# Kernel tuning notes

Measured on AMD Instinct MI355X. Metric: run time of the kernel, lower is better.

The kernel has to match this reference:

```python
import jax, jax.numpy as jnp
import numpy as np

B, LP, LQ, H = 16, 1024, 1024, 1024


def setup_inputs() -> dict:
    key = jax.random.key(0)
    k1, k2, k3 = jax.random.split(key, 3)
    p = jax.random.normal(k1, (B, LP, H), dtype=jnp.float32)
    q = jax.random.normal(k2, (B, LQ, H), dtype=jnp.float32)
    # Dense(hidden_size) kernel + bias (glorot-ish scale)
    W_key = jax.random.normal(k3, (H, H), dtype=jnp.float32) / np.sqrt(H)
    b_key = jnp.zeros((H,), dtype=jnp.float32)
    return {"p": p, "q": q, "W_key": W_key, "b_key": b_key}


def reference(p, q, W_key, b_key):
    # keys = Dense(q): [B, LQ, H]
    keys = jnp.einsum("bqh,hk->bqk", q, W_key) + b_key
    # attention scores p @ keys^T (no scaling): [B, LP, LQ]
    scores = jnp.einsum("bph,bqh->bpq", p, keys)
    attn = jax.nn.softmax(scores, axis=-1)
    # q reused as values; relu on output: [B, LP, H]
    out = jax.nn.relu(jnp.einsum("bpq,bqh->bph", attn, q))
    return out
```

## Files before the change

kernel.cpp:

```cpp
#include <hip/hip_runtime.h>
#include <hip/hip_bf16.h>

#define B_N 16
#define LP_N 1024
#define LQ_N 1024
#define H_N 1024

typedef unsigned short u16;
typedef __attribute__((ext_vector_type(8))) _Float16 f16x8;
typedef __attribute__((ext_vector_type(4))) float f32x4;

__device__ __forceinline__ u16 f2h(float x) {
    _Float16 h = (_Float16)x;
    return *(u16*)&h;
}
__device__ __forceinline__ float h2f(u16 u) {
    _Float16 h;
    *(u16*)&h = u;
    return (float)h;
}

__device__ __forceinline__ void load_lds16(const u16* g, u16* l) {
    __builtin_amdgcn_global_load_lds(
        (const __attribute__((address_space(1))) void*)g,
        (__attribute__((address_space(3))) void*)l, 16, 0, 0);
}

#define MFMA_F16(a, b, c) __builtin_amdgcn_mfma_f32_16x16x32_f16(a, b, c, 0, 0, 0)
#define VMW0()  asm volatile("s_waitcnt vmcnt(0)" ::: "memory")
#define VMW4()  asm volatile("s_waitcnt vmcnt(4)" ::: "memory")
#define LGKM8() asm volatile("s_waitcnt lgkmcnt(8)" ::: "memory")
#define LGKM0() asm volatile("s_waitcnt lgkmcnt(0)" ::: "memory")
#define SCHB()  __builtin_amdgcn_sched_barrier(0)
#define SBAR()  __builtin_amdgcn_s_barrier()

template<bool SPLIT, int EPI>
__launch_bounds__(512, 2)
__global__ void gemm2t(const u16* __restrict__ Ahi, const u16* __restrict__ Alo,
                       const u16* __restrict__ Bm,
                       const float* __restrict__ bias,
                       float* __restrict__ Cf, u16* __restrict__ Ch,
                       int N, int gn, int gmn,
                       long long sA, long long sB, long long sC)
{
    constexpr int REG  = 8192;
    constexpr int O_AL = REG;
    constexpr int O_B  = SPLIT ? 2 * REG : REG;
    constexpr int BUF  = SPLIT ? 3 * REG : 2 * REG;
    __shared__ __align__(16) u16 lds[2 * BUF];

    const int tid  = threadIdx.x;
    const int lane = tid & 63;
    const int wv   = tid >> 6;
    const int wr   = wv >> 2, wc = wv & 3;

    const int d   = blockIdx.x;
    const int cpx = gridDim.x >> 3;
    const int swz = (d & 7) * cpx + (d >> 3);
    const long long z = swz / gmn;
    const int r_  = swz % gmn;
    const int bm  = (r_ / gn) * 256;
    const int bn  = (r_ % gn) * 256;

    const char* pAh = (const char*)(Ahi + z * sA);
    const char* pAl = (const char*)(Alo + z * sA);
    const char* pB  = (const char*)(Bm + z * sB);

    const int r0 = tid >> 2;
    const int xc = (tid & 3) ^ ((r0 >> 1) & 3);
    const long long aof = (long long)(bm + r0) * 2048 + xc * 16;
    const long long bof = (long long)(bn + r0) * 2048 + xc * 16;
    const long long ao2 = aof + 128 * 2048;
    const long long bo2 = bof + 128 * 2048;
    const int d0 = tid * 8;
    const int d1 = d0 + 4096;

    int offA[8], offB[4];
#pragma unroll
    for (int i = 0; i < 8; ++i) {
        const int r = wr * 128 + i * 16 + (lane & 15);
        offA[i] = r * 32 + ((((lane >> 4) ^ (r >> 1)) & 3) << 3);
    }
#pragma unroll
    for (int j = 0; j < 4; ++j) {
        const int r = wc * 64 + j * 16 + (lane & 15);
        offB[j] = r * 32 + ((((lane >> 4) ^ (r >> 1)) & 3) << 3);
    }

    f32x4 acc[8][4];
#pragma unroll
    for (int i = 0; i < 8; ++i)
#pragma unroll
        for (int j = 0; j < 4; ++j)
            acc[i][j] = (f32x4){0.f, 0.f, 0.f, 0.f};

#define STG(NB, KB) do {                                                      \
        load_lds16((const u16*)(pAh + aof + (KB)), lds + (NB) + d0);          \
        load_lds16((const u16*)(pAh + ao2 + (KB)), lds + (NB) + d1);          \
        load_lds16((const u16*)(pB + bof + (KB)), lds + (NB) + O_B + d0);     \
        load_lds16((const u16*)(pB + bo2 + (KB)), lds + (NB) + O_B + d1);     \
        if constexpr (SPLIT) {                                                \
            load_lds16((const u16*)(pAl + aof + (KB)), lds + (NB) + O_AL + d0); \
            load_lds16((const u16*)(pAl + ao2 + (KB)), lds + (NB) + O_AL + d1); \
        }                                                                     \
    } while (0)

#define TERM(AF, BF) do {                                                     \
        __builtin_amdgcn_s_setprio(1);                                        \
        _Pragma("unroll")                                                     \
        for (int i = 0; i < 8; ++i)                                           \
            _Pragma("unroll")                                                 \
            for (int j = 0; j < 4; ++j)                                       \
                acc[i][j] = MFMA_F16(AF[i], BF[j], acc[i][j]);                \
        __builtin_amdgcn_s_setprio(0);                                        \
    } while (0)

    constexpr int NT = 32;

    STG(0, 0);

    for (int t = 0; t < NT; ++t) {
        const int cb = (t & 1) ? BUF : 0;
        const int nb = (t & 1) ? 0 : BUF;
        const long long kb = (long long)(t + 1) * 64;

        VMW0();
        SBAR();
        f16x8 b[4], ah[8], al[8];
#pragma unroll
        for (int j = 0; j < 4; ++j)
            b[j] = *(const f16x8*)(lds + cb + O_B + offB[j]);
#pragma unroll
        for (int i = 0; i < 8; ++i)
            ah[i] = *(const f16x8*)(lds + cb + offA[i]);
        if constexpr (SPLIT) {
#pragma unroll
            for (int i = 0; i < 8; ++i)
                al[i] = *(const f16x8*)(lds + cb + O_AL + offA[i]);
        }
        if (t + 1 < NT) STG(nb, kb);
        if constexpr (SPLIT) { LGKM8(); } else { LGKM0(); }
        SCHB();
        TERM(ah, b);
        if constexpr (SPLIT) {
            LGKM0(); SCHB();
            TERM(al, b);
        }
    }
#undef STG
#undef TERM

    const long long Cbase = z * sC;
#pragma unroll
    for (int i = 0; i < 8; ++i) {
        const int row0 = bm + wr * 128 + i * 16 + ((lane >> 4) << 2);
#pragma unroll
        for (int j = 0; j < 4; ++j) {
            const int col = bn + wc * 64 + j * 16 + (lane & 15);
#pragma unroll
            for (int e = 0; e < 4; ++e) {
                const float v = acc[i][j][e];
                const long long idx = Cbase + (long long)(row0 + e) * N + col;
                if constexpr (EPI == 0) {
                    Cf[idx] = v;
                } else if constexpr (EPI == 1) {
                    Ch[idx] = f2h(v + bias[col]);
                } else {
                    Cf[idx] = fmaxf(v, 0.f);
                }
            }
        }
    }
}

template<int EPI>
__launch_bounds__(512, 2)
__global__ void gemm_p8(const u16* __restrict__ Am, const u16* __restrict__ Bm,
                        float* __restrict__ Cf,
                        int N, int gn, int gmn,
                        long long sA, long long sB, long long sC)
{
    constexpr int OB    = 16384;
    constexpr int BUFSZ = 32768;
    __shared__ __align__(16) u16 lds[2 * BUFSZ];

    const int tid  = threadIdx.x;
    const int lane = tid & 63;
    const int wv   = tid >> 6;
    const int wr   = wv >> 2, wc = wv & 3;

    const int d   = blockIdx.x;
    const int cpx = gridDim.x >> 3;
    const int swz = (d & 7) * cpx + (d >> 3);
    const long long z = swz / gmn;
    const int r_  = swz % gmn;
    const int bm  = (r_ / gn) * 256;
    const int bn  = (r_ % gn) * 256;

    const char* pA = (const char*)(Am + z * sA);
    const char* pB = (const char*)(Bm + z * sB);

    const int rr  = tid >> 3;
    const int xcv = (tid & 7) ^ (rr & 7);
    long long aofs[4], bofs[4];
#pragma unroll
    for (int j = 0; j < 4; ++j) {
        aofs[j] = (long long)(bm + rr + j * 64) * 2048 + xcv * 16;
        bofs[j] = (long long)(bn + rr + j * 64) * 2048 + xcv * 16;
    }

    int offA[8][2], offB[4][2];
#pragma unroll
    for (int i = 0; i < 8; ++i) {
        const int r = wr * 128 + i * 16 + (lane & 15);
#pragma unroll
        for (int s = 0; s < 2; ++s)
            offA[i][s] = r * 64 + ((((s * 4 + (lane >> 4)) ^ r) & 7) << 3);
    }
#pragma unroll
    for (int j = 0; j < 4; ++j) {
        const int r = wc * 64 + j * 16 + (lane & 15);
#pragma unroll
        for (int s = 0; s < 2; ++s)
            offB[j][s] = OB + r * 64 + ((((s * 4 + (lane >> 4)) ^ r) & 7) << 3);
    }

    f32x4 acc[8][4];
#pragma unroll
    for (int i = 0; i < 8; ++i)
#pragma unroll
        for (int j = 0; j < 4; ++j)
            acc[i][j] = (f32x4){0.f, 0.f, 0.f, 0.f};

    f16x8 bb[4][2];

#define STA(NB, J, KB) load_lds16((const u16*)(pA + aofs[J] + (KB)), \
                                  lds + (NB) + tid * 8 + (J) * 4096)
#define STB(NB, J, KB) load_lds16((const u16*)(pB + bofs[J] + (KB)), \
                                  lds + (NB) + OB + tid * 8 + (J) * 4096)
#define RD_BB(CB) do {                                                        \
        _Pragma("unroll")                                                     \
        for (int j = 0; j < 4; ++j) {                                         \
            bb[j][0] = *(const f16x8*)(lds + (CB) + offB[j][0]);              \
            bb[j][1] = *(const f16x8*)(lds + (CB) + offB[j][1]);              \
        }                                                                     \
    } while (0)
#define PHASE(CB, I0, FIRST, STAGES, WAITST) do {                             \
        if (FIRST) RD_BB(CB);                                                 \
        f16x8 a00 = *(const f16x8*)(lds + (CB) + offA[(I0)][0]);              \
        f16x8 a01 = *(const f16x8*)(lds + (CB) + offA[(I0)][1]);              \
        f16x8 a10 = *(const f16x8*)(lds + (CB) + offA[(I0) + 1][0]);          \
        f16x8 a11 = *(const f16x8*)(lds + (CB) + offA[(I0) + 1][1]);          \
        STAGES;                                                               \
        if (FIRST) LGKM8();                                                   \
        SBAR();                                                               \
        LGKM0(); SCHB();                                                      \
        __builtin_amdgcn_s_setprio(1);                                        \
        _Pragma("unroll")                                                     \
        for (int j = 0; j < 4; ++j) {                                         \
            acc[(I0)][j]     = MFMA_F16(a00, bb[j][0], acc[(I0)][j]);         \
            acc[(I0)][j]     = MFMA_F16(a01, bb[j][1], acc[(I0)][j]);         \
            acc[(I0) + 1][j] = MFMA_F16(a10, bb[j][0], acc[(I0) + 1][j]);     \
            acc[(I0) + 1][j] = MFMA_F16(a11, bb[j][1], acc[(I0) + 1][j]);     \
        }                                                                     \
        __builtin_amdgcn_s_setprio(0);                                        \
        WAITST;                                                               \
        SBAR();                                                               \
    } while (0)

    constexpr int NT2 = 8;

    STB(0, 0, 0); STB(0, 1, 0); STB(0, 2, 0); STB(0, 3, 0);
    STA(0, 0, 0); STA(0, 1, 0); STA(0, 2, 0); STA(0, 3, 0);
    STB(BUFSZ, 0, 128); STB(BUFSZ, 1, 128); STB(BUFSZ, 2, 128); STB(BUFSZ, 3, 128);
    VMW4();
    SBAR();

    for (int it = 0; it < NT2; ++it) {
        const long long kb1 = (long long)(2 * it + 1) * 128;
        const long long kb2 = (long long)(2 * it + 2) * 128;
        const long long kb3 = (long long)(2 * it + 3) * 128;
        const bool st2 = (it + 1) < NT2;

        PHASE(0, 0, true,  { STA(BUFSZ, 0, kb1); STA(BUFSZ, 1, kb1); }, );
        PHASE(0, 2, false, { STA(BUFSZ, 2, kb1); STA(BUFSZ, 3, kb1); }, );
        PHASE(0, 4, false, { if (st2) { STB(0, 0, kb2); STB(0, 1, kb2); } }, );
        PHASE(0, 6, false, { if (st2) { STB(0, 2, kb2); STB(0, 3, kb2); } },
              { if (st2) { VMW4(); } else { VMW0(); } });
        PHASE(BUFSZ, 0, true,  { if (st2) { STA(0, 0, kb2); STA(0, 1, kb2); } }, );
        PHASE(BUFSZ, 2, false, { if (st2) { STA(0, 2, kb2); STA(0, 3, kb2); } }, );
        PHASE(BUFSZ, 4, false, { if (st2) { STB(BUFSZ, 0, kb3); STB(BUFSZ, 1, kb3); } }, );
        PHASE(BUFSZ, 6, false, { if (st2) { STB(BUFSZ, 2, kb3); STB(BUFSZ, 3, kb3); } },
              { if (st2) VMW4(); });
    }
#undef STA
#undef STB
#undef RD_BB
#undef PHASE

    const long long Cbase = z * sC;
#pragma unroll
    for (int i = 0; i < 8; ++i) {
        const int row0 = bm + wr * 128 + i * 16 + ((lane >> 4) << 2);
#pragma unroll
        for (int j = 0; j < 4; ++j) {
            const int col = bn + wc * 64 + j * 16 + (lane & 15);
#pragma unroll
            for (int e = 0; e < 4; ++e) {
                const float v = acc[i][j][e];
                const long long idx = Cbase + (long long)(row0 + e) * N + col;
                if constexpr (EPI == 0) Cf[idx] = v;
                else                    Cf[idx] = fmaxf(v, 0.f);
            }
        }
    }
}

__global__ void cvt_f16(const float* __restrict__ in, u16* __restrict__ o16,
                        long long n4)
{
    const long long i = (long long)blockIdx.x * 256 + threadIdx.x;
    if (i >= n4) return;
    const float4 v = ((const float4*)in)[i];
    ushort4 h;
    h.x = f2h(v.x); h.y = f2h(v.y); h.z = f2h(v.z); h.w = f2h(v.w);
    ((ushort4*)o16)[i] = h;
}

__global__ void fuse_cvt_q(const float* __restrict__ q, u16* __restrict__ hi,
                           u16* __restrict__ lo, u16* __restrict__ thi)
{
    __shared__ float t[32][33];
    const long long z = blockIdx.z;
    const long long base = z * 1048576;
    const int r0 = blockIdx.y * 32, c0 = blockIdx.x * 32;
    for (int j = threadIdx.y; j < 32; j += 8) {
        const float v = q[base + (long long)(r0 + j) * 1024 + c0 + threadIdx.x];
        t[j][threadIdx.x] = v;
        const long long o = base + (long long)(r0 + j) * 1024 + c0 + threadIdx.x;
        const u16 h = f2h(v);
        hi[o] = h;
        lo[o] = f2h(v - h2f(h));
    }
    __syncthreads();
    for (int j = threadIdx.y; j < 32; j += 8)
        thi[base + (long long)(c0 + j) * 1024 + r0 + threadIdx.x] = f2h(t[threadIdx.x][j]);
}

__global__ void transpose_cvt_w(const float* __restrict__ in, u16* __restrict__ hi)
{
    __shared__ float t[32][33];
    const int r0 = blockIdx.y * 32, c0 = blockIdx.x * 32;
    for (int j = threadIdx.y; j < 32; j += 8)
        t[j][threadIdx.x] = in[(long long)(r0 + j) * 1024 + c0 + threadIdx.x];
    __syncthreads();
    for (int j = threadIdx.y; j < 32; j += 8)
        hi[(long long)(c0 + j) * 1024 + r0 + threadIdx.x] = f2h(t[threadIdx.x][j]);
}

__global__ void softmax_f16(const float* __restrict__ S, u16* __restrict__ A)
{
    const long long row = blockIdx.x;
    const float* r = S + row * (long long)LQ_N;
    const int t = threadIdx.x;
    float4 v = ((const float4*)r)[t];

    float m = fmaxf(fmaxf(v.x, v.y), fmaxf(v.z, v.w));
#pragma unroll
    for (int off = 32; off > 0; off >>= 1)
        m = fmaxf(m, __shfl_xor(m, off));

    __shared__ float red[4];
    const int lane = t & 63, wid = t >> 6;
    if (lane == 0) red[wid] = m;
    __syncthreads();
    m = fmaxf(fmaxf(red[0], red[1]), fmaxf(red[2], red[3]));
    __syncthreads();

    v.x = __expf(v.x - m); v.y = __expf(v.y - m);
    v.z = __expf(v.z - m); v.w = __expf(v.w - m);
    float s = v.x + v.y + v.z + v.w;
#pragma unroll
    for (int off = 32; off > 0; off >>= 1)
        s += __shfl_xor(s, off);
    if (lane == 0) red[wid] = s;
    __syncthreads();
    s = red[0] + red[1] + red[2] + red[3];

    const float inv = 1.0f / s;
    ushort4 o;
    o.x = f2h(v.x * inv); o.y = f2h(v.y * inv);
    o.z = f2h(v.z * inv); o.w = f2h(v.w * inv);
    ((ushort4*)(A + row * (long long)LQ_N))[t] = o;
}

#define BM 128
#define BN 128
#define BK 8
#define TM 8
#define TN 8

template<bool TRANSB, bool BIAS, bool RELU>
__launch_bounds__(256)
__global__ void gemm_k(const float* __restrict__ A, const float* __restrict__ Bmat,
                       const float* __restrict__ bias, float* __restrict__ C,
                       int M, int N, int K,
                       long long sA, long long sB, long long sC)
{
    __shared__ float As[BK][BM];
    __shared__ float Bs[BK][BN];
    const int tid = threadIdx.x;
    const int tx = tid & 15;
    const int ty = tid >> 4;
    const int bn = blockIdx.x * BN;
    const int bm = blockIdx.y * BM;
    const long long z = blockIdx.z;
    A += z * sA; Bmat += z * sB; C += z * sC;
    float acc[TM][TN];
#pragma unroll
    for (int i = 0; i < TM; i++)
#pragma unroll
        for (int j = 0; j < TN; j++) acc[i][j] = 0.f;
    const int arow = tid >> 1;
    const int acol = (tid & 1) * 4;
    const int bk_n = tid >> 5;
    const int bn_n = (tid & 31) * 4;
    for (int k0 = 0; k0 < K; k0 += BK) {
        float4 a4 = *(const float4*)&A[(long long)(bm + arow) * K + k0 + acol];
        As[acol + 0][arow] = a4.x; As[acol + 1][arow] = a4.y;
        As[acol + 2][arow] = a4.z; As[acol + 3][arow] = a4.w;
        if (TRANSB) {
            float4 b4 = *(const float4*)&Bmat[(long long)(bn + arow) * K + k0 + acol];
            Bs[acol + 0][arow] = b4.x; Bs[acol + 1][arow] = b4.y;
            Bs[acol + 2][arow] = b4.z; Bs[acol + 3][arow] = b4.w;
        } else {
            float4 b4 = *(const float4*)&Bmat[(long long)(k0 + bk_n) * N + bn + bn_n];
            *(float4*)&Bs[bk_n][bn_n] = b4;
        }
        __syncthreads();
#pragma unroll
        for (int k = 0; k < BK; k++) {
            float a[TM], b[TN];
            *(float4*)&a[0] = *(const float4*)&As[k][ty * TM];
            *(float4*)&a[4] = *(const float4*)&As[k][ty * TM + 4];
            *(float4*)&b[0] = *(const float4*)&Bs[k][tx * TN];
            *(float4*)&b[4] = *(const float4*)&Bs[k][tx * TN + 4];
#pragma unroll
            for (int i = 0; i < TM; i++)
#pragma unroll
                for (int j = 0; j < TN; j++)
                    acc[i][j] = fmaf(a[i], b[j], acc[i][j]);
        }
        __syncthreads();
    }
#pragma unroll
    for (int i = 0; i < TM; i++) {
        const int row = bm + ty * TM + i;
#pragma unroll
        for (int j = 0; j < TN; j += 4) {
            const int col = bn + tx * TN + j;
            float4 v;
            v.x = acc[i][j + 0]; v.y = acc[i][j + 1];
            v.z = acc[i][j + 2]; v.w = acc[i][j + 3];
            if (BIAS) {
                v.x += bias[col + 0]; v.y += bias[col + 1];
                v.z += bias[col + 2]; v.w += bias[col + 3];
            }
            if (RELU) {
                v.x = fmaxf(v.x, 0.f); v.y = fmaxf(v.y, 0.f);
                v.z = fmaxf(v.z, 0.f); v.w = fmaxf(v.w, 0.f);
            }
            *(float4*)&C[(long long)row * N + col] = v;
        }
    }
}

__global__ void softmax_k(float* __restrict__ S)
{
    const long long row = blockIdx.x;
    float* r = S + row * (long long)LQ_N;
    const int t = threadIdx.x;
    float4 v = ((float4*)r)[t];
    float m = fmaxf(fmaxf(v.x, v.y), fmaxf(v.z, v.w));
#pragma unroll
    for (int off = 32; off > 0; off >>= 1)
        m = fmaxf(m, __shfl_xor(m, off));
    __shared__ float red[4];
    const int lane = t & 63, wid = t >> 6;
    if (lane == 0) red[wid] = m;
    __syncthreads();
    m = fmaxf(fmaxf(red[0], red[1]), fmaxf(red[2], red[3]));
    __syncthreads();
    v.x = __expf(v.x - m); v.y = __expf(v.y - m);
    v.z = __expf(v.z - m); v.w = __expf(v.w - m);
    float s = v.x + v.y + v.z + v.w;
#pragma unroll
    for (int off = 32; off > 0; off >>= 1)
        s += __shfl_xor(s, off);
    if (lane == 0) red[wid] = s;
    __syncthreads();
    s = red[0] + red[1] + red[2] + red[3];
    const float inv = 1.0f / s;
    v.x *= inv; v.y *= inv; v.z *= inv; v.w *= inv;
    ((float4*)r)[t] = v;
}

extern "C" void kernel_launch(void* const* d_in, const int* in_sizes, int n_in,
                              void* d_out, int out_size, void* d_ws, size_t ws_size,
                              hipStream_t stream)
{
    const float* p    = (const float*)d_in[0];
    const float* q    = (const float*)d_in[1];
    const float* W    = (const float*)d_in[2];
    const float* bias = (const float*)d_in[3];
    float* out = (float*)d_out;

    const size_t MB32 = 33554432ull;
    const size_t NEED = 5 * MB32 + 2097152ull;

    if (ws_size >= NEED) {
        char* w = (char*)d_ws;
        u16* p16   = (u16*)(w + 0 * MB32);
        u16* q_hi  = (u16*)(w + 1 * MB32);
        u16* q_lo  = (u16*)(w + 2 * MB32);
        u16* keys  = (u16*)(w + 3 * MB32);
        u16* qT    = (u16*)(w + 4 * MB32);
        u16* Wt    = (u16*)(w + 5 * MB32);
        float* scores = (float*)(w + 1 * MB32);
        u16* attn     = (u16*)(w + 0 * MB32);

        const long long n4 = (long long)B_N * LQ_N * H_N / 4;
        cvt_f16<<<dim3((unsigned)(n4 / 256)), 256, 0, stream>>>(p, p16, n4);
        fuse_cvt_q<<<dim3(32, 32, B_N), dim3(32, 8), 0, stream>>>(q, q_hi, q_lo, qT);
        transpose_cvt_w<<<dim3(32, 32, 1), dim3(32, 8), 0, stream>>>(W, Wt);

        gemm2t<true, 1><<<256, 512, 0, stream>>>(
            q_hi, q_lo, Wt, bias, nullptr, keys,
            H_N, 4, 256, 0, 0, 0);

        gemm_p8<0><<<256, 512, 0, stream>>>(
            p16, keys, scores,
            LQ_N, 4, 16,
            (long long)LP_N * H_N, (long long)LQ_N * H_N, (long long)LP_N * LQ_N);

        softmax_f16<<<B_N * LP_N, 256, 0, stream>>>(scores, attn);

        gemm_p8<2><<<256, 512, 0, stream>>>(
            attn, qT, out,
            H_N, 4, 16,
            (long long)LP_N * LQ_N, (long long)H_N * LQ_N, (long long)LP_N * H_N);
    } else {
        float* keys   = (float*)d_ws;
        float* scores = keys + (long long)B_N * LQ_N * H_N;

        gemm_k<false, true, false><<<dim3(H_N / BN, (B_N * LQ_N) / BM, 1), 256, 0, stream>>>(
            q, W, bias, keys, B_N * LQ_N, H_N, H_N, 0, 0, 0);
        gemm_k<true, false, false><<<dim3(LQ_N / BN, LP_N / BM, B_N), 256, 0, stream>>>(
            p, keys, nullptr, scores, LP_N, LQ_N, H_N,
            (long long)LP_N * H_N, (long long)LQ_N * H_N, (long long)LP_N * LQ_N);
        softmax_k<<<B_N * LP_N, 256, 0, stream>>>(scores);
        gemm_k<false, false, true><<<dim3(H_N / BN, LP_N / BM, B_N), 256, 0, stream>>>(
            scores, q, nullptr, out, LP_N, H_N, LQ_N,
            (long long)LP_N * LQ_N, (long long)LQ_N * H_N, (long long)LP_N * H_N);
    }
}
```

Measured before the change: 221.4 us.

## Rewrite keys GEMM with phased LDS pipeline interleaving loads and MFMAs

Replaces the templated split-precision GEMM used for the keys projection with a dedicated kernel that splits each K-tile into four phases over pairs of A row-fragments. Global-to-LDS stages for the next tile are issued piecemeal inside the phases, with partial vmcnt waits and barriers, instead of all at once before compute. This is meant to overlap memory traffic with MFMA work and to lower register pressure by holding fewer fragments live. It adds more barriers per tile and depends on fine-grained wait counts being correct.

Result: no change. 222.3 us (+0.4%).

```diff
diff --git a/kernel.cpp b/kernel.cpp
--- a/kernel.cpp
+++ b/kernel.cpp
@@ -28,26 +28,23 @@
 
 #define MFMA_F16(a, b, c) __builtin_amdgcn_mfma_f32_16x16x32_f16(a, b, c, 0, 0, 0)
 #define VMW0()  asm volatile("s_waitcnt vmcnt(0)" ::: "memory")
+#define VMW2()  asm volatile("s_waitcnt vmcnt(2)" ::: "memory")
 #define VMW4()  asm volatile("s_waitcnt vmcnt(4)" ::: "memory")
 #define LGKM8() asm volatile("s_waitcnt lgkmcnt(8)" ::: "memory")
 #define LGKM0() asm volatile("s_waitcnt lgkmcnt(0)" ::: "memory")
 #define SCHB()  __builtin_amdgcn_sched_barrier(0)
 #define SBAR()  __builtin_amdgcn_s_barrier()
 
-template<bool SPLIT, int EPI>
 __launch_bounds__(512, 2)
-__global__ void gemm2t(const u16* __restrict__ Ahi, const u16* __restrict__ Alo,
-                       const u16* __restrict__ Bm,
-                       const float* __restrict__ bias,
-                       float* __restrict__ Cf, u16* __restrict__ Ch,
-                       int N, int gn, int gmn,
-                       long long sA, long long sB, long long sC)
-{
-    constexpr int REG  = 8192;
-    constexpr int O_AL = REG;
-    constexpr int O_B  = SPLIT ? 2 * REG : REG;
-    constexpr int BUF  = SPLIT ? 3 * REG : 2 * REG;
-    __shared__ __align__(16) u16 lds[2 * BUF];
+__global__ void gemm1_p8(const u16* __restrict__ Ahi, const u16* __restrict__ Alo,
+                         const u16* __restrict__ Bm,
+                         const float* __restrict__ bias, u16* __restrict__ Ch,
+                         int N, int gn, int gmn)
+{
+    constexpr int O_AL  = 8192;
+    constexpr int O_B   = 16384;
+    constexpr int BUFSZ = 24576;
+    __shared__ __align__(16) u16 lds[2 * BUFSZ];
 
     const int tid  = threadIdx.x;
     const int lane = tid & 63;
@@ -62,9 +59,9 @@
     const int bm  = (r_ / gn) * 256;
     const int bn  = (r_ % gn) * 256;
 
-    const char* pAh = (const char*)(Ahi + z * sA);
-    const char* pAl = (const char*)(Alo + z * sA);
-    const char* pB  = (const char*)(Bm + z * sB);
+    const char* pAh = (const char*)Ahi;
+    const char* pAl = (const char*)Alo;
+    const char* pB  = (const char*)Bm;
 
     const int r0 = tid >> 2;
     const int xc = (tid & 3) ^ ((r0 >> 1) & 3);
@@ -84,7 +81,7 @@
 #pragma unroll
     for (int j = 0; j < 4; ++j) {
         const int r = wc * 64 + j * 16 + (lane & 15);
-        offB[j] = r * 32 + ((((lane >> 4) ^ (r >> 1)) & 3) << 3);
+        offB[j] = O_B + r * 32 + ((((lane >> 4) ^ (r >> 1)) & 3) << 3);
     }
 
     f32x4 acc[8][4];
@@ -94,63 +91,72 @@
         for (int j = 0; j < 4; ++j)
             acc[i][j] = (f32x4){0.f, 0.f, 0.f, 0.f};
 
-#define STG(NB, KB) do {                                                      \
-        load_lds16((const u16*)(pAh + aof + (KB)), lds + (NB) + d0);          \
-        load_lds16((const u16*)(pAh + ao2 + (KB)), lds + (NB) + d1);          \
-        load_lds16((const u16*)(pB + bof + (KB)), lds + (NB) + O_B + d0);     \
-        load_lds16((const u16*)(pB + bo2 + (KB)), lds + (NB) + O_B + d1);     \
-        if constexpr (SPLIT) {                                                \
-            load_lds16((const u16*)(pAl + aof + (KB)), lds + (NB) + O_AL + d0); \
-            load_lds16((const u16*)(pAl + ao2 + (KB)), lds + (NB) + O_AL + d1); \
-        }                                                                     \
+    f16x8 bb[4];
+
+#define SAH(NB, KB) do { load_lds16((const u16*)(pAh + aof + (KB)), lds + (NB) + d0);          \
+                         load_lds16((const u16*)(pAh + ao2 + (KB)), lds + (NB) + d1); } while (0)
+#define SAL(NB, KB) do { load_lds16((const u16*)(pAl + aof + (KB)), lds + (NB) + O_AL + d0);   \
+                         load_lds16((const u16*)(pAl + ao2 + (KB)), lds + (NB) + O_AL + d1); } while (0)
+#define SB_(NB, KB) do { load_lds16((const u16*)(pB + bof + (KB)), lds + (NB) + O_B + d0);     \
+                         load_lds16((const u16*)(pB + bo2 + (KB)), lds + (NB) + O_B + d1); } while (0)
+#define RD_BB(CB) do {                                                        \
+        _Pragma("unroll")                                                     \
+        for (int j = 0; j < 4; ++j)                                           \
+            bb[j] = *(const f16x8*)(lds + (CB) + offB[j]);                    \
     } while (0)
-
-#define TERM(AF, BF) do {                                                     \
+#define PHASE(CB, I0, FIRST, STAGES, WAITST) do {                             \
+        if (FIRST) RD_BB(CB);                                                 \
+        f16x8 ah0 = *(const f16x8*)(lds + (CB) + offA[(I0)]);                 \
+        f16x8 ah1 = *(const f16x8*)(lds + (CB) + offA[(I0) + 1]);             \
+        f16x8 al0 = *(const f16x8*)(lds + (CB) + O_AL + offA[(I0)]);          \
+        f16x8 al1 = *(const f16x8*)(lds + (CB) + O_AL + offA[(I0) + 1]);      \
+        STAGES;                                                               \
+        SBAR();                                                               \
+        LGKM0(); SCHB();                                                      \
         __builtin_amdgcn_s_setprio(1);                                        \
         _Pragma("unroll")                                                     \
-        for (int i = 0; i < 8; ++i)                                           \
-            _Pragma("unroll")                                                 \
-            for (int j = 0; j < 4; ++j)                                       \
-                acc[i][j] = MFMA_F16(AF[i], BF[j], acc[i][j]);                \
+        for (int j = 0; j < 4; ++j) {                                         \
+            acc[(I0)][j]     = MFMA_F16(ah0, bb[j], acc[(I0)][j]);            \
+            acc[(I0)][j]     = MFMA_F16(al0, bb[j], acc[(I0)][j]);            \
+            acc[(I0) + 1][j] = MFMA_F16(ah1, bb[j], acc[(I0) + 1][j]);        \
+            acc[(I0) + 1][j] = MFMA_F16(al1, bb[j], acc[(I0) + 1][j]);        \
+        }                                                                     \
         __builtin_amdgcn_s_setprio(0);                                        \
+        WAITST;                                                               \
+        SBAR();                                                               \
     } while (0)
 
-    constexpr int NT = 32;
-
-    STG(0, 0);
-
-    for (int t = 0; t < NT; ++t) {
-        const int cb = (t & 1) ? BUF : 0;
-        const int nb = (t & 1) ? 0 : BUF;
-        const long long kb = (long long)(t + 1) * 64;
-
-        VMW0();
-        SBAR();
-        f16x8 b[4], ah[8], al[8];
-#pragma unroll
-        for (int j = 0; j < 4; ++j)
-            b[j] = *(const f16x8*)(lds + cb + O_B + offB[j]);
-#pragma unroll
-        for (int i = 0; i < 8; ++i)
-            ah[i] = *(const f16x8*)(lds + cb + offA[i]);
-        if constexpr (SPLIT) {
-#pragma unroll
-            for (int i = 0; i < 8; ++i)
-                al[i] = *(const f16x8*)(lds + cb + O_AL + offA[i]);
-        }
-        if (t + 1 < NT) STG(nb, kb);
-        if constexpr (SPLIT) { LGKM8(); } else { LGKM0(); }
-        SCHB();
-        TERM(ah, b);
-        if constexpr (SPLIT) {
-            LGKM0(); SCHB();
-            TERM(al, b);
-        }
-    }
-#undef STG
-#undef TERM
-
-    const long long Cbase = z * sC;
+    constexpr int NT2 = 16;
+
+    SB_(0, 0); SAH(0, 0); SAL(0, 0);
+    SB_(BUFSZ, 64);
+    VMW2();
+    SBAR();
+
+    for (int it = 0; it < NT2; ++it) {
+        const long long kb1 = (long long)(2 * it + 1) * 64;
+        const long long kb2 = (long long)(2 * it + 2) * 64;
+        const long long kb3 = (long long)(2 * it + 3) * 64;
+        const bool st2 = (it + 1) < NT2;
+
+        PHASE(0, 0, true,  { SAH(BUFSZ, kb1); }, );
+        PHASE(0, 2, false, { SAL(BUFSZ, kb1); }, );
+        PHASE(0, 4, false, { if (st2) SB_(0, kb2); }, );
+        PHASE(0, 6, false, { },
+              { if (st2) { VMW2(); } else { VMW0(); } });
+        PHASE(BUFSZ, 0, true,  { if (st2) SAH(0, kb2); }, );
+        PHASE(BUFSZ, 2, false, { if (st2) SAL(0, kb2); }, );
+        PHASE(BUFSZ, 4, false, { if (st2) SB_(BUFSZ, kb3); }, );
+        PHASE(BUFSZ, 6, false, { },
+              { if (st2) VMW2(); });
+    }
+#undef SAH
+#undef SAL
+#undef SB_
+#undef RD_BB
+#undef PHASE
+
+    (void)z;
 #pragma unroll
     for (int i = 0; i < 8; ++i) {
         const int row0 = bm + wr * 128 + i * 16 + ((lane >> 4) << 2);
@@ -159,15 +165,8 @@
             const int col = bn + wc * 64 + j * 16 + (lane & 15);
 #pragma unroll
             for (int e = 0; e < 4; ++e) {
-                const float v = acc[i][j][e];
-                const long long idx = Cbase + (long long)(row0 + e) * N + col;
-                if constexpr (EPI == 0) {
-                    Cf[idx] = v;
-                } else if constexpr (EPI == 1) {
-                    Ch[idx] = f2h(v + bias[col]);
-                } else {
-                    Cf[idx] = fmaxf(v, 0.f);
-                }
+                const long long idx = (long long)(row0 + e) * N + col;
+                Ch[idx] = f2h(acc[i][j][e] + bias[col]);
             }
         }
     }
@@ -534,9 +533,9 @@
         fuse_cvt_q<<<dim3(32, 32, B_N), dim3(32, 8), 0, stream>>>(q, q_hi, q_lo, qT);
         transpose_cvt_w<<<dim3(32, 32, 1), dim3(32, 8), 0, stream>>>(W, Wt);
 
-        gemm2t<true, 1><<<256, 512, 0, stream>>>(
-            q_hi, q_lo, Wt, bias, nullptr, keys,
-            H_N, 4, 256, 0, 0, 0);
+        gemm1_p8<<<256, 512, 0, stream>>>(
+            q_hi, q_lo, Wt, bias, keys,
+            H_N, 4, 256);
 
         gemm_p8<0><<<256, 512, 0, stream>>>(
             p16, keys, scores,
```
